# Kernel optimization log

Measured on AMD Instinct MI355X. Metric: run time of the kernel, lower is better.

## Reference

```python
import jax, jax.numpy as jnp
import numpy as np

B = 1048576
INDIM = 10
DIM = 32
LAYERS = 4
MODES = DIM // 2 + 1  # 17 rfft modes


def setup_inputs() -> dict:
    key = jax.random.key(0)
    ks = jax.random.split(key, 10)
    scale = 1.0 / (DIM * DIM)
    inp = {
        "x": jax.random.normal(ks[0], (B, INDIM), dtype=jnp.float32),
        # stem: Linear(indim, dim), stored as [in, out]
        "stem_W": jax.random.normal(ks[1], (INDIM, DIM), dtype=jnp.float32) / np.sqrt(INDIM),
        "stem_b": jnp.zeros((DIM,), dtype=jnp.float32),
        # per-layer complex spectral weights, stored as real/imag parts [L, modes, modes]
        "fno_wr": scale * jax.random.uniform(ks[2], (LAYERS, MODES, MODES), dtype=jnp.float32),
        "fno_wi": scale * jax.random.uniform(ks[3], (LAYERS, MODES, MODES), dtype=jnp.float32),
        # per-layer proj: Linear(dim, dim), stored as [L, in, out]
        "proj_W": jax.random.normal(ks[4], (LAYERS, DIM, DIM), dtype=jnp.float32) / np.sqrt(DIM),
        "proj_b": jnp.zeros((LAYERS, DIM), dtype=jnp.float32),
        # head: Linear(dim, indim)
        "head_W": jax.random.normal(ks[5], (DIM, INDIM), dtype=jnp.float32) / np.sqrt(DIM),
        "head_b": jnp.zeros((INDIM,), dtype=jnp.float32),
    }
    return inp


def reference(x, stem_W, stem_b, fno_wr, fno_wi, proj_W, proj_b, head_W, head_b):
    # stem
    h = x @ stem_W + stem_b  # [B, DIM]
    for i in range(LAYERS):
        w = fno_wr[i] + 1j * fno_wi[i]  # [MODES, MODES] complex64
        hf = jnp.fft.rfft(h, axis=-1)  # [B, MODES] complex
        # complex linear mix of modes (bias=False since condition_num=0)
        x1 = jnp.fft.irfft(jnp.einsum('bi,io->bo', hf, w), axis=-1)  # [B, DIM]
        x2 = h @ proj_W[i] + proj_b[i]  # [B, DIM]
        h = jax.nn.silu(x1 + x2)
    return h @ head_W + head_b  # [B, INDIM]
```

## Files before the change

### kernel.cpp

```cpp
#include <hip/hip_runtime.h>
#include <math.h>

#define INDIM 10
#define DIM 32
#define LAYERS 4
#define MODES 17

#define LOG2E 1.4426950408889634f
#define LN2   0.6931471805599453f

#define WS_FRAG_OFF 0
#define WS_BIAS_OFF 11264

typedef _Float16 f16;
typedef _Float16 f16x8 __attribute__((ext_vector_type(8)));
typedef float f32x16 __attribute__((ext_vector_type(16)));
typedef unsigned u32x2 __attribute__((ext_vector_type(2)));

union BU { f16x8 v; unsigned u[4]; };
union CU { f32x16 v; float4 q[4]; };

__global__ void fno_prep(const float* __restrict__ wr,
                         const float* __restrict__ wi,
                         const float* __restrict__ projW,
                         const float* __restrict__ stemW,
                         const float* __restrict__ headW,
                         const float* __restrict__ stemB,
                         const float* __restrict__ projB,
                         const float* __restrict__ headB,
                         f16* __restrict__ frag,
                         float* __restrict__ bias2) {
    const int l  = blockIdx.x;
    const int tx = threadIdx.x;
    const int j  = tx & 31;
    const int n  = tx >> 5;

    __shared__ float ct[32], st[32];
    if (tx < 32) {
        float ang = (2.0f * 3.14159265358979323846f / 32.0f) * (float)tx;
        ct[tx] = cosf(ang);
        st[tx] = sinf(ang);
    }
    __syncthreads();

    const float* lwr = wr + l * MODES * MODES;
    const float* lwi = wi + l * MODES * MODES;

    float acc = 0.0f;
    for (int o = 0; o < MODES; ++o) {
        float re = 0.0f, im = 0.0f;
        for (int m = 0; m < MODES; ++m) {
            int t = (m * n) & 31;
            float c = ct[t], s = st[t];
            float a = lwr[m * MODES + o];
            float b = lwi[m * MODES + o];
            re += c * a + s * b;
            im += c * b - s * a;
        }
        int t2 = (o * j) & 31;
        float f = (o == 0 || o == 16) ? 1.0f : 2.0f;
        acc += f * (re * ct[t2] - im * st[t2]);
    }
    acc = acc * (1.0f / 32.0f) + projW[(l * DIM + n) * DIM + j];

    const float wscale = (l == 0) ? LOG2E : 1.0f;
    const int kc = n >> 4;
    const int G  = (n >> 3) & 1;
    const int e  = n & 7;
    const int ln = G * 32 + j;
    frag[((l * 2 + kc) * 64 + ln) * 8 + e] = (f16)(wscale * acc);

    if (l == 0) {
        if (tx < 64) {
            const int lnn = tx;
            const int c2  = lnn & 31;
            const int G2  = lnn >> 5;
#pragma unroll
            for (int ee = 0; ee < 8; ++ee) {
                int k = 8 * G2 + ee;
                frag[(8 * 64 + lnn) * 8 + ee] =
                    (f16)(k < INDIM ? stemW[k * DIM + c2] : 0.0f);
            }
#pragma unroll
            for (int kcc = 0; kcc < 2; ++kcc)
#pragma unroll
                for (int ee = 0; ee < 8; ++ee) {
                    int k = 16 * kcc + 8 * G2 + ee;
                    frag[((9 + kcc) * 64 + lnn) * 8 + ee] =
                        (f16)(c2 < INDIM ? LN2 * headW[k * INDIM + c2] : 0.0f);
                }
        }
        if (tx < 32) {
#pragma unroll
            for (int f = 0; f < 6; ++f) {
                float v;
                if (f == 0)      v = stemB[tx];
                else if (f <= 4) v = LOG2E * projB[(f - 1) * DIM + tx];
                else             v = (tx < INDIM) ? headB[tx] : 0.0f;
                bias2[f * 32 + tx] = v;
            }
        }
    }
}

__device__ __forceinline__ float exp2_fast(float x) {
#if __has_builtin(__builtin_amdgcn_exp2f)
    return __builtin_amdgcn_exp2f(x);
#else
    return exp2f(x);
#endif
}

__device__ __forceinline__ unsigned pk2(float a, float b) {
    auto h2 = __builtin_amdgcn_cvt_pkrtz(a, b);
    return __builtin_bit_cast(unsigned, h2);
}

__device__ __forceinline__ void pswap(unsigned& a, unsigned& b) {
#if __has_builtin(__builtin_amdgcn_permlane32_swap)
    u32x2 r = __builtin_amdgcn_permlane32_swap(a, b, false, false);
    a = r[0];
    b = r[1];
#else
    asm("v_permlane32_swap_b32 %0, %1" : "+v"(a), "+v"(b));
    __builtin_amdgcn_sched_barrier(0);
#endif
}

template <bool SILU>
__device__ __forceinline__ void pack_exchange_dual(const f32x16& DA, const f32x16& DB,
                                                   BU& a0, BU& a1, BU& b0, BU& b1) {
    float sA[16], sB[16];
    if (SILU) {
        float uA[16], uB[16];
#pragma unroll
        for (int r = 0; r < 16; ++r) uA[r] = exp2_fast(-DA[r]);
#pragma unroll
        for (int r = 0; r < 16; ++r) uB[r] = exp2_fast(-DB[r]);
#pragma unroll
        for (int r = 0; r < 16; ++r) uA[r] = 1.0f + uA[r];
#pragma unroll
        for (int r = 0; r < 16; ++r) uB[r] = 1.0f + uB[r];
#pragma unroll
        for (int r = 0; r < 16; ++r) uA[r] = __builtin_amdgcn_rcpf(uA[r]);
#pragma unroll
        for (int r = 0; r < 16; ++r) uB[r] = __builtin_amdgcn_rcpf(uB[r]);
#pragma unroll
        for (int r = 0; r < 16; ++r) sA[r] = DA[r] * uA[r];
#pragma unroll
        for (int r = 0; r < 16; ++r) sB[r] = DB[r] * uB[r];
    } else {
#pragma unroll
        for (int r = 0; r < 16; ++r) { sA[r] = DA[r]; sB[r] = DB[r]; }
    }

    unsigned qa0 = pk2(sA[0],  sA[1]);
    unsigned qa1 = pk2(sA[2],  sA[3]);
    unsigned qa2 = pk2(sA[4],  sA[5]);
    unsigned qa3 = pk2(sA[6],  sA[7]);
    unsigned qa4 = pk2(sA[8],  sA[9]);
    unsigned qa5 = pk2(sA[10], sA[11]);
    unsigned qa6 = pk2(sA[12], sA[13]);
    unsigned qa7 = pk2(sA[14], sA[15]);
    unsigned qb0 = pk2(sB[0],  sB[1]);
    unsigned qb1 = pk2(sB[2],  sB[3]);
    unsigned qb2 = pk2(sB[4],  sB[5]);
    unsigned qb3 = pk2(sB[6],  sB[7]);
    unsigned qb4 = pk2(sB[8],  sB[9]);
    unsigned qb5 = pk2(sB[10], sB[11]);
    unsigned qb6 = pk2(sB[12], sB[13]);
    unsigned qb7 = pk2(sB[14], sB[15]);
    pswap(qa0, qa2); pswap(qa1, qa3); pswap(qa4, qa6); pswap(qa5, qa7);
    pswap(qb0, qb2); pswap(qb1, qb3); pswap(qb4, qb6); pswap(qb5, qb7);
    a0.u[0] = qa0; a0.u[1] = qa1; a0.u[2] = qa2; a0.u[3] = qa3;
    a1.u[0] = qa4; a1.u[1] = qa5; a1.u[2] = qa6; a1.u[3] = qa7;
    b0.u[0] = qb0; b0.u[1] = qb1; b0.u[2] = qb2; b0.u[3] = qb3;
    b1.u[0] = qb4; b1.u[1] = qb5; b1.u[2] = qb6; b1.u[3] = qb7;
}

__device__ __forceinline__ f32x16 ld_bias(const float* sbias, int stage, int G) {
    CU c;
#pragma unroll
    for (int rq = 0; rq < 4; ++rq)
        c.q[rq] = *(const float4*)&sbias[stage * 32 + rq * 8 + G * 4];
    return c.v;
}

__device__ __forceinline__ f16x8 ld_frag(const f16* sfrag, int f, int ln) {
    return *(const f16x8*)&sfrag[(f * 64 + ln) * 8];
}

template <bool GUARD>
__device__ __forceinline__ BU load_x(const float* __restrict__ x, long rb,
                                     int c, int G, int nrows) {
    BU b;
    b.u[0] = 0; b.u[1] = 0; b.u[2] = 0; b.u[3] = 0;
    const long r = rb + c;
    if (!GUARD || r < nrows) {
        const float* xp = x + r * INDIM;
        if (G == 0) {
            float2 p0 = *(const float2*)(xp + 0);
            float2 p1 = *(const float2*)(xp + 2);
            float2 p2 = *(const float2*)(xp + 4);
            float2 p3 = *(const float2*)(xp + 6);
            b.u[0] = pk2(p0.x, p0.y);
            b.u[1] = pk2(p1.x, p1.y);
            b.u[2] = pk2(p2.x, p2.y);
            b.u[3] = pk2(p3.x, p3.y);
        } else {
            float2 p4 = *(const float2*)(xp + 8);
            b.u[0] = pk2(p4.x, p4.y);
        }
    }
    return b;
}

template <bool GUARD>
__device__ __forceinline__ void store_o(float* __restrict__ out, long rb,
                                        int c, int G, int nrows, const f32x16& Dh) {
    const long r = rb + c;
    if (!GUARD || r < nrows) {
        float* op = out + r * INDIM;
        if (G == 0) {
            *(float2*)(op + 0) = make_float2(Dh[0], Dh[1]);
            *(float2*)(op + 2) = make_float2(Dh[2], Dh[3]);
            *(float2*)(op + 8) = make_float2(Dh[4], Dh[5]);
        } else {
            *(float2*)(op + 4) = make_float2(Dh[0], Dh[1]);
            *(float2*)(op + 6) = make_float2(Dh[2], Dh[3]);
        }
    }
}

template <bool GUARD>
__global__ __launch_bounds__(256, 4) void fno_main(
    const float* __restrict__ x,
    const f16*  __restrict__ fragbuf,
    const float* __restrict__ bias2,
    float* __restrict__ out,
    int nrows) {

    __shared__ __align__(16) f16 sfrag[11 * 64 * 8];
    __shared__ __align__(16) float sbias[6 * 32];

    {
        const int tid = threadIdx.x;
        uint4* dv = (uint4*)sfrag;
        const uint4* sv = (const uint4*)fragbuf;
#pragma unroll
        for (int i = 0; i < 3; ++i) {
            int idx = tid + i * 256;
            if (idx < 704) dv[idx] = sv[idx];
        }
        if (tid < 48) ((float4*)sbias)[tid] = ((const float4*)bias2)[tid];
    }
    __syncthreads();

    const int tid = threadIdx.x;
    const int w   = tid >> 6;
    const int ln  = tid & 63;
    const int c   = ln & 31;
    const int G   = ln >> 5;

    const long rbA = (long)blockIdx.x * 256 + (long)w * 64;
    const long rbB = rbA + 32;

    BU bxA = load_x<GUARD>(x, rbA, c, G, nrows);
    BU bxB = load_x<GUARD>(x, rbB, c, G, nrows);
    f32x16 cb = ld_bias(sbias, 0, G);
    f16x8 as = ld_frag(sfrag, 8, ln);
    f32x16 DA = __builtin_amdgcn_mfma_f32_32x32x16_f16(as, bxA.v, cb, 0, 0, 0);
    f32x16 DB = __builtin_amdgcn_mfma_f32_32x32x16_f16(as, bxB.v, cb, 0, 0, 0);
    cb = ld_bias(sbias, 1, G);

    BU a0, a1, b0, b1;
    pack_exchange_dual<false>(DA, DB, a0, a1, b0, b1);

#pragma unroll
    for (int l = 0; l < LAYERS; ++l) {
        f16x8 w0 = ld_frag(sfrag, 2 * l, ln);
        f16x8 w1 = ld_frag(sfrag, 2 * l + 1, ln);
        f32x16 tA = __builtin_amdgcn_mfma_f32_32x32x16_f16(w0, a0.v, cb, 0, 0, 0);
        f32x16 tB = __builtin_amdgcn_mfma_f32_32x32x16_f16(w0, b0.v, cb, 0, 0, 0);
        tA = __builtin_amdgcn_mfma_f32_32x32x16_f16(w1, a1.v, tA, 0, 0, 0);
        tB = __builtin_amdgcn_mfma_f32_32x32x16_f16(w1, b1.v, tB, 0, 0, 0);
        cb = ld_bias(sbias, (l < LAYERS - 1) ? (2 + l) : 5, G);
        pack_exchange_dual<true>(tA, tB, a0, a1, b0, b1);
    }

    f16x8 ah0 = ld_frag(sfrag, 9, ln);
    f16x8 ah1 = ld_frag(sfrag, 10, ln);
    f32x16 HA = __builtin_amdgcn_mfma_f32_32x32x16_f16(ah0, a0.v, cb, 0, 0, 0);
    f32x16 HB = __builtin_amdgcn_mfma_f32_32x32x16_f16(ah0, b0.v, cb, 0, 0, 0);
    HA = __builtin_amdgcn_mfma_f32_32x32x16_f16(ah1, a1.v, HA, 0, 0, 0);
    HB = __builtin_amdgcn_mfma_f32_32x32x16_f16(ah1, b1.v, HB, 0, 0, 0);

    store_o<GUARD>(out, rbA, c, G, nrows, HA);
    store_o<GUARD>(out, rbB, c, G, nrows, HB);
}

extern "C" void kernel_launch(void* const* d_in, const int* in_sizes, int n_in,
                              void* d_out, int out_size, void* d_ws, size_t ws_size,
                              hipStream_t stream) {
    const float* x      = (const float*)d_in[0];
    const float* stemW  = (const float*)d_in[1];
    const float* stemB  = (const float*)d_in[2];
    const float* fno_wr = (const float*)d_in[3];
    const float* fno_wi = (const float*)d_in[4];
    const float* projW  = (const float*)d_in[5];
    const float* projB  = (const float*)d_in[6];
    const float* headW  = (const float*)d_in[7];
    const float* headB  = (const float*)d_in[8];
    float* out = (float*)d_out;

    f16*   frag  = (f16*)((char*)d_ws + WS_FRAG_OFF);
    float* bias2 = (float*)((char*)d_ws + WS_BIAS_OFF);

    const int nrows = in_sizes[0] / INDIM;

    fno_prep<<<LAYERS, 1024, 0, stream>>>(fno_wr, fno_wi, projW, stemW, headW,
                                          stemB, projB, headB, frag, bias2);

    const int rows_per_block = 256;
    const int nblk = (nrows + rows_per_block - 1) / rows_per_block;
    if (nrows % rows_per_block == 0)
        fno_main<false><<<nblk, 256, 0, stream>>>(x, frag, bias2, out, nrows);
    else
        fno_main<true><<<nblk, 256, 0, stream>>>(x, frag, bias2, out, nrows);
}
```

Before: 60.77 us.

## Process one 32-row tile per wave instead of two to raise occupancy

Each wave now handles a single 32-row MFMA tile rather than two interleaved tiles (A/B), halving rows per block to 128 and doubling the grid. Launch bounds rise from 4 to 6 waves-per-EU hint to allow more resident waves with the reduced register footprint. This trades away the instruction-level parallelism of two independent MFMA chains per wave for more wave-level parallelism. It also repeats the per-block shared-memory fragment load across twice as many blocks.

Result: faster. 57.82 us (-4.8%).

```diff
diff --git a/kernel.cpp b/kernel.cpp
--- a/kernel.cpp
+++ b/kernel.cpp
@@ -128,54 +128,36 @@
 }
 
 template <bool SILU>
-__device__ __forceinline__ void pack_exchange_dual(const f32x16& DA, const f32x16& DB,
-                                                   BU& a0, BU& a1, BU& b0, BU& b1) {
-    float sA[16], sB[16];
+__device__ __forceinline__ void pack_exchange(const f32x16& D, BU& b0, BU& b1) {
+    float s[16];
     if (SILU) {
-        float uA[16], uB[16];
-#pragma unroll
-        for (int r = 0; r < 16; ++r) uA[r] = exp2_fast(-DA[r]);
-#pragma unroll
-        for (int r = 0; r < 16; ++r) uB[r] = exp2_fast(-DB[r]);
-#pragma unroll
-        for (int r = 0; r < 16; ++r) uA[r] = 1.0f + uA[r];
-#pragma unroll
-        for (int r = 0; r < 16; ++r) uB[r] = 1.0f + uB[r];
-#pragma unroll
-        for (int r = 0; r < 16; ++r) uA[r] = __builtin_amdgcn_rcpf(uA[r]);
-#pragma unroll
-        for (int r = 0; r < 16; ++r) uB[r] = __builtin_amdgcn_rcpf(uB[r]);
-#pragma unroll
-        for (int r = 0; r < 16; ++r) sA[r] = DA[r] * uA[r];
-#pragma unroll
-        for (int r = 0; r < 16; ++r) sB[r] = DB[r] * uB[r];
+        float u[16];
+#pragma unroll
+        for (int r = 0; r < 16; ++r) u[r] = exp2_fast(-D[r]);
+#pragma unroll
+        for (int r = 0; r < 16; ++r) u[r] = 1.0f + u[r];
+#pragma unroll
+        for (int r = 0; r < 16; ++r) u[r] = __builtin_amdgcn_rcpf(u[r]);
+#pragma unroll
+        for (int r = 0; r < 16; ++r) s[r] = D[r] * u[r];
     } else {
 #pragma unroll
-        for (int r = 0; r < 16; ++r) { sA[r] = DA[r]; sB[r] = DB[r]; }
-    }
-
-    unsigned qa0 = pk2(sA[0],  sA[1]);
-    unsigned qa1 = pk2(sA[2],  sA[3]);
-    unsigned qa2 = pk2(sA[4],  sA[5]);
-    unsigned qa3 = pk2(sA[6],  sA[7]);
-    unsigned qa4 = pk2(sA[8],  sA[9]);
-    unsigned qa5 = pk2(sA[10], sA[11]);
-    unsigned qa6 = pk2(sA[12], sA[13]);
-    unsigned qa7 = pk2(sA[14], sA[15]);
-    unsigned qb0 = pk2(sB[0],  sB[1]);
-    unsigned qb1 = pk2(sB[2],  sB[3]);
-    unsigned qb2 = pk2(sB[4],  sB[5]);
-    unsigned qb3 = pk2(sB[6],  sB[7]);
-    unsigned qb4 = pk2(sB[8],  sB[9]);
-    unsigned qb5 = pk2(sB[10], sB[11]);
-    unsigned qb6 = pk2(sB[12], sB[13]);
-    unsigned qb7 = pk2(sB[14], sB[15]);
-    pswap(qa0, qa2); pswap(qa1, qa3); pswap(qa4, qa6); pswap(qa5, qa7);
-    pswap(qb0, qb2); pswap(qb1, qb3); pswap(qb4, qb6); pswap(qb5, qb7);
-    a0.u[0] = qa0; a0.u[1] = qa1; a0.u[2] = qa2; a0.u[3] = qa3;
-    a1.u[0] = qa4; a1.u[1] = qa5; a1.u[2] = qa6; a1.u[3] = qa7;
-    b0.u[0] = qb0; b0.u[1] = qb1; b0.u[2] = qb2; b0.u[3] = qb3;
-    b1.u[0] = qb4; b1.u[1] = qb5; b1.u[2] = qb6; b1.u[3] = qb7;
+        for (int r = 0; r < 16; ++r) s[r] = D[r];
+    }
+    unsigned q0 = pk2(s[0],  s[1]);
+    unsigned q1 = pk2(s[2],  s[3]);
+    unsigned q2 = pk2(s[4],  s[5]);
+    unsigned q3 = pk2(s[6],  s[7]);
+    unsigned q4 = pk2(s[8],  s[9]);
+    unsigned q5 = pk2(s[10], s[11]);
+    unsigned q6 = pk2(s[12], s[13]);
+    unsigned q7 = pk2(s[14], s[15]);
+    pswap(q0, q2);
+    pswap(q1, q3);
+    pswap(q4, q6);
+    pswap(q5, q7);
+    b0.u[0] = q0; b0.u[1] = q1; b0.u[2] = q2; b0.u[3] = q3;
+    b1.u[0] = q4; b1.u[1] = q5; b1.u[2] = q6; b1.u[3] = q7;
 }
 
 __device__ __forceinline__ f32x16 ld_bias(const float* sbias, int stage, int G) {
@@ -233,7 +215,7 @@
 }
 
 template <bool GUARD>
-__global__ __launch_bounds__(256, 4) void fno_main(
+__global__ __launch_bounds__(256, 6) void fno_main(
     const float* __restrict__ x,
     const f16*  __restrict__ fragbuf,
     const float* __restrict__ bias2,
@@ -262,41 +244,33 @@
     const int c   = ln & 31;
     const int G   = ln >> 5;
 
-    const long rbA = (long)blockIdx.x * 256 + (long)w * 64;
-    const long rbB = rbA + 32;
-
-    BU bxA = load_x<GUARD>(x, rbA, c, G, nrows);
-    BU bxB = load_x<GUARD>(x, rbB, c, G, nrows);
+    const long rb = (long)blockIdx.x * 128 + (long)w * 32;
+
+    BU bx = load_x<GUARD>(x, rb, c, G, nrows);
+    f16x8 as = ld_frag(sfrag, 8, ln);
     f32x16 cb = ld_bias(sbias, 0, G);
-    f16x8 as = ld_frag(sfrag, 8, ln);
-    f32x16 DA = __builtin_amdgcn_mfma_f32_32x32x16_f16(as, bxA.v, cb, 0, 0, 0);
-    f32x16 DB = __builtin_amdgcn_mfma_f32_32x32x16_f16(as, bxB.v, cb, 0, 0, 0);
-    cb = ld_bias(sbias, 1, G);
-
-    BU a0, a1, b0, b1;
-    pack_exchange_dual<false>(DA, DB, a0, a1, b0, b1);
+    f32x16 D = __builtin_amdgcn_mfma_f32_32x32x16_f16(as, bx.v, cb, 0, 0, 0);
+
+    BU b0, b1;
+    pack_exchange<false>(D, b0, b1);
 
 #pragma unroll
     for (int l = 0; l < LAYERS; ++l) {
         f16x8 w0 = ld_frag(sfrag, 2 * l, ln);
         f16x8 w1 = ld_frag(sfrag, 2 * l + 1, ln);
-        f32x16 tA = __builtin_amdgcn_mfma_f32_32x32x16_f16(w0, a0.v, cb, 0, 0, 0);
-        f32x16 tB = __builtin_amdgcn_mfma_f32_32x32x16_f16(w0, b0.v, cb, 0, 0, 0);
-        tA = __builtin_amdgcn_mfma_f32_32x32x16_f16(w1, a1.v, tA, 0, 0, 0);
-        tB = __builtin_amdgcn_mfma_f32_32x32x16_f16(w1, b1.v, tB, 0, 0, 0);
-        cb = ld_bias(sbias, (l < LAYERS - 1) ? (2 + l) : 5, G);
-        pack_exchange_dual<true>(tA, tB, a0, a1, b0, b1);
+        cb = ld_bias(sbias, 1 + l, G);
+        f32x16 t = __builtin_amdgcn_mfma_f32_32x32x16_f16(w0, b0.v, cb, 0, 0, 0);
+        t = __builtin_amdgcn_mfma_f32_32x32x16_f16(w1, b1.v, t, 0, 0, 0);
+        pack_exchange<true>(t, b0, b1);
     }
 
     f16x8 ah0 = ld_frag(sfrag, 9, ln);
     f16x8 ah1 = ld_frag(sfrag, 10, ln);
-    f32x16 HA = __builtin_amdgcn_mfma_f32_32x32x16_f16(ah0, a0.v, cb, 0, 0, 0);
-    f32x16 HB = __builtin_amdgcn_mfma_f32_32x32x16_f16(ah0, b0.v, cb, 0, 0, 0);
-    HA = __builtin_amdgcn_mfma_f32_32x32x16_f16(ah1, a1.v, HA, 0, 0, 0);
-    HB = __builtin_amdgcn_mfma_f32_32x32x16_f16(ah1, b1.v, HB, 0, 0, 0);
-
-    store_o<GUARD>(out, rbA, c, G, nrows, HA);
-    store_o<GUARD>(out, rbB, c, G, nrows, HB);
+    cb = ld_bias(sbias, 5, G);
+    f32x16 H = __builtin_amdgcn_mfma_f32_32x32x16_f16(ah0, b0.v, cb, 0, 0, 0);
+    H = __builtin_amdgcn_mfma_f32_32x32x16_f16(ah1, b1.v, H, 0, 0, 0);
+
+    store_o<GUARD>(out, rb, c, G, nrows, H);
 }
 
 extern "C" void kernel_launch(void* const* d_in, const int* in_sizes, int n_in,
@@ -321,7 +295,7 @@
     fno_prep<<<LAYERS, 1024, 0, stream>>>(fno_wr, fno_wi, projW, stemW, headW,
                                           stemB, projB, headB, frag, bias2);
 
-    const int rows_per_block = 256;
+    const int rows_per_block = 128;
     const int nblk = (nrows + rows_per_block - 1) / rows_per_block;
     if (nrows % rows_per_block == 0)
         fno_main<false><<<nblk, 256, 0, stream>>>(x, frag, bias2, out, nrows);
```
